# Performance work log

Measured on AMD Instinct MI355X. Metric: run time of the kernel, lower is better.

## Reference

```python
import jax, jax.numpy as jnp
import numpy as np
import math

N_HEADS = 16

def setup_inputs() -> dict:
    key = jax.random.key(0)
    ks = jax.random.split(key, 5)
    B, S, D = 4, 2048, 1024
    scale = 0.02
    return {
        "x": jax.random.normal(ks[0], (B, S, D), dtype=jnp.float32),
        "w_in": jax.random.normal(ks[1], (D, 3 * D), dtype=jnp.float32) * scale,
        "b_in": jax.random.normal(ks[2], (3 * D,), dtype=jnp.float32) * scale,
        "w_out": jax.random.normal(ks[3], (D, D), dtype=jnp.float32) * scale,
        "b_out": jax.random.normal(ks[4], (D,), dtype=jnp.float32) * scale,
    }

def reference(x, w_in, b_in, w_out, b_out):
    B, S, D = x.shape
    H = N_HEADS
    dh = D // H
    qkv = x @ w_in + b_in                      # [B,S,3D]
    q, k, v = jnp.split(qkv, 3, axis=-1)
    # [B,S,D] -> [B,H,S,dh]
    q = q.reshape(B, S, H, dh).transpose(0, 2, 1, 3)
    k = k.reshape(B, S, H, dh).transpose(0, 2, 1, 3)
    v = v.reshape(B, S, H, dh).transpose(0, 2, 1, 3)
    scores = jnp.einsum("bhqd,bhkd->bhqk", q, k) / math.sqrt(dh)
    causal = jnp.tril(jnp.ones((S, S), dtype=bool))  # allow k <= q
    scores = jnp.where(causal, scores, -jnp.inf)
    wei = jax.nn.softmax(scores, axis=-1)
    out = jnp.einsum("bhqk,bhkd->bhqd", wei, v)      # [B,H,S,dh]
    out = out.transpose(0, 2, 1, 3).reshape(B, S, D)
    return out @ w_out + b_out
```

## Files before the change

kernel.cpp:

```cpp
#include <hip/hip_runtime.h>

typedef unsigned short u16;
typedef unsigned int   u32;
typedef float  f32x4  __attribute__((ext_vector_type(4)));
typedef __bf16 bf16x8 __attribute__((ext_vector_type(8)));
typedef __bf16 bf16x4 __attribute__((ext_vector_type(4)));
typedef short  s16x4  __attribute__((ext_vector_type(4)));
typedef unsigned short u16x8 __attribute__((ext_vector_type(8)));
typedef unsigned int   u32x4 __attribute__((ext_vector_type(4)));

__device__ __forceinline__ u16 f2bf(float f) {
  u32 u = __builtin_bit_cast(u32, f);
  u = (u + 0x7fffu + ((u >> 16) & 1u)) >> 16;
  return (u16)u;
}

__device__ __forceinline__ void gload_lds16(const void* g, void* l) {
  __builtin_amdgcn_global_load_lds(
      (const __attribute__((address_space(1))) void*)g,
      (__attribute__((address_space(3))) void*)l, 16, 0, 0);
}

#define LGKM0()  asm volatile("s_waitcnt lgkmcnt(0)" ::: "memory")
#define VMCNT6() asm volatile("s_waitcnt vmcnt(6)" ::: "memory")
#define VMCNT0() asm volatile("s_waitcnt vmcnt(0)" ::: "memory")

__global__ __launch_bounds__(256) void conv_f32_bf16(
    const float* __restrict__ in, u16* __restrict__ out, int n8) {
  int i = blockIdx.x * 256 + threadIdx.x;
  if (i >= n8) return;
  const float4* p = (const float4*)in;
  float4 a = p[2 * i], b = p[2 * i + 1];
  u16x8 r;
  r[0] = f2bf(a.x); r[1] = f2bf(a.y); r[2] = f2bf(a.z); r[3] = f2bf(a.w);
  r[4] = f2bf(b.x); r[5] = f2bf(b.y); r[6] = f2bf(b.z); r[7] = f2bf(b.w);
  ((u16x8*)out)[i] = r;
}

__global__ __launch_bounds__(256) void conv_transpose(
    const float* __restrict__ in, u16* __restrict__ out, int K, int N) {
  __shared__ float tile[64][65];
  int nb = N >> 6;
  int tk = blockIdx.x / nb, tn = blockIdx.x % nb;
  int t = threadIdx.x;
  int kl = t >> 4, n4 = (t & 15) * 4;
#pragma unroll
  for (int i = 0; i < 4; ++i) {
    int k = kl + 16 * i;
    float4 v = *(const float4*)(in + (size_t)(tk * 64 + k) * N + tn * 64 + n4);
    tile[k][n4] = v.x; tile[k][n4 + 1] = v.y; tile[k][n4 + 2] = v.z; tile[k][n4 + 3] = v.w;
  }
  __syncthreads();
  int nl = t >> 4, k4 = (t & 15) * 4;
#pragma unroll
  for (int i = 0; i < 4; ++i) {
    int n = nl + 16 * i;
    ushort4 o;
    o.x = f2bf(tile[k4 + 0][n]); o.y = f2bf(tile[k4 + 1][n]);
    o.z = f2bf(tile[k4 + 2][n]); o.w = f2bf(tile[k4 + 3][n]);
    *(ushort4*)(out + (size_t)(tn * 64 + n) * K + tk * 64 + k4) = o;
  }
}

template <int OUT_BF16, int SCALE_Q>
__global__ __launch_bounds__(512, 2) void gemm8p(
    const u16* __restrict__ A, const u16* __restrict__ Bt,
    const float* __restrict__ bias, void* __restrict__ C,
    int M, int N, int K) {
  __shared__ __align__(16) char smem[2][49152];
  int tid = threadIdx.x, w = tid >> 6, lane = tid & 63;
  int g = lane >> 4, l15 = lane & 15, l7 = lane & 7, l8 = lane >> 3;
  int wm = w >> 2, wn = w & 3;
  int cpx = (int)gridDim.x >> 3;
  int bid = (blockIdx.x & 7) * cpx + (blockIdx.x >> 3);
  int nblk = N >> 7;
  int bm = bid / nblk, bn = bid % nblk;
  int m0 = bm << 8, n0 = bn << 7;

  auto stageA = [&](int buf, int kt, int h) {
#pragma unroll
    for (int i = 0; i < 2; ++i) {
      int row = h * 128 + w * 16 + i * 8 + l8;
      const u16* src = A + (size_t)(m0 + row) * K + kt * 64 + 8 * (l7 ^ (row & 7));
      gload_lds16(src, &smem[buf][(h * 128 + w * 16 + i * 8) * 128]);
    }
  };
  auto stageB = [&](int buf, int kt, int h) {
    int row = h * 64 + w * 8 + l8;
    const u16* src = Bt + (size_t)(n0 + row) * K + kt * 64 + 8 * (l7 ^ (row & 7));
    gload_lds16(src, &smem[buf][32768 + (h * 64 + w * 8) * 128]);
  };
  auto ldA = [&](int buf, int mh, int mi, int kk) -> bf16x8 {
    int row = mh * 128 + wm * 64 + mi * 16 + l15;
    return *(const bf16x8*)&smem[buf][row * 128 + (((kk * 4 + g) * 16) ^ ((row & 7) << 4))];
  };
  auto ldB = [&](int buf, int nh, int kk) -> bf16x8 {
    int row = nh * 64 + wn * 16 + l15;
    return *(const bf16x8*)&smem[buf][32768 + row * 128 + (((kk * 4 + g) * 16) ^ ((row & 7) << 4))];
  };

  f32x4 acc[2][4][2];
#pragma unroll
  for (int mh = 0; mh < 2; ++mh)
#pragma unroll
    for (int mi = 0; mi < 4; ++mi)
#pragma unroll
      for (int nh = 0; nh < 2; ++nh) acc[mh][mi][nh] = f32x4{0.f, 0.f, 0.f, 0.f};

  const int NT = K >> 6;
#pragma unroll
  for (int t = 0; t < 2; ++t) {
    stageB(t, t, 0); stageA(t, t, 0); stageB(t, t, 1); stageA(t, t, 1);
  }
  VMCNT6();
  __builtin_amdgcn_s_barrier();

  for (int t = 0; t < NT; ++t) {
    int b = t & 1;
    bool pf = (t + 2) < NT;
    bf16x8 af[4][2], b0f[2], b1f[2];

#pragma unroll
    for (int mi = 0; mi < 4; ++mi)
#pragma unroll
      for (int kk = 0; kk < 2; ++kk) af[mi][kk] = ldA(b, 0, mi, kk);
#pragma unroll
    for (int kk = 0; kk < 2; ++kk) b0f[kk] = ldB(b, 0, kk);
    LGKM0();
    __builtin_amdgcn_s_barrier();
    if (pf) stageB(b, t + 2, 0);
    __builtin_amdgcn_s_setprio(1);
#pragma unroll
    for (int mi = 0; mi < 4; ++mi)
#pragma unroll
      for (int kk = 0; kk < 2; ++kk)
        acc[0][mi][0] = __builtin_amdgcn_mfma_f32_16x16x32_bf16(af[mi][kk], b0f[kk], acc[0][mi][0], 0, 0, 0);
    __builtin_amdgcn_s_setprio(0);

#pragma unroll
    for (int kk = 0; kk < 2; ++kk) b1f[kk] = ldB(b, 1, kk);
    LGKM0();
    __builtin_amdgcn_s_barrier();
    if (pf) stageA(b, t + 2, 0);
    __builtin_amdgcn_s_setprio(1);
#pragma unroll
    for (int mi = 0; mi < 4; ++mi)
#pragma unroll
      for (int kk = 0; kk < 2; ++kk)
        acc[0][mi][1] = __builtin_amdgcn_mfma_f32_16x16x32_bf16(af[mi][kk], b1f[kk], acc[0][mi][1], 0, 0, 0);
    __builtin_amdgcn_s_setprio(0);

#pragma unroll
    for (int mi = 0; mi < 4; ++mi)
#pragma unroll
      for (int kk = 0; kk < 2; ++kk) af[mi][kk] = ldA(b, 1, mi, kk);
    LGKM0();
    __builtin_amdgcn_s_barrier();
    if (pf) stageB(b, t + 2, 1);
    __builtin_amdgcn_s_setprio(1);
#pragma unroll
    for (int mi = 0; mi < 4; ++mi)
#pragma unroll
      for (int kk = 0; kk < 2; ++kk)
        acc[1][mi][1] = __builtin_amdgcn_mfma_f32_16x16x32_bf16(af[mi][kk], b1f[kk], acc[1][mi][1], 0, 0, 0);
    __builtin_amdgcn_s_setprio(0);

    if (pf) stageA(b, t + 2, 1);
    __builtin_amdgcn_s_setprio(1);
#pragma unroll
    for (int mi = 0; mi < 4; ++mi)
#pragma unroll
      for (int kk = 0; kk < 2; ++kk)
        acc[1][mi][0] = __builtin_amdgcn_mfma_f32_16x16x32_bf16(af[mi][kk], b0f[kk], acc[1][mi][0], 0, 0, 0);
    __builtin_amdgcn_s_setprio(0);

    if (t < NT - 1) {
      if (pf) VMCNT6(); else VMCNT0();
      __builtin_amdgcn_s_barrier();
    }
  }

#pragma unroll
  for (int nh = 0; nh < 2; ++nh) {
    int col = n0 + nh * 64 + wn * 16 + l15;
    float bv = bias[col];
    float sc = (SCALE_Q && col < 1024) ? 0.18033688011112042f : 1.0f;
#pragma unroll
    for (int mh = 0; mh < 2; ++mh)
#pragma unroll
      for (int mi = 0; mi < 4; ++mi) {
        int rowb = m0 + mh * 128 + wm * 64 + mi * 16 + g * 4;
#pragma unroll
        for (int r = 0; r < 4; ++r) {
          float v = (acc[mh][mi][nh][r] + bv) * sc;
          if (OUT_BF16)
            ((u16*)C)[(size_t)(rowb + r) * N + col] = f2bf(v);
          else
            ((float*)C)[(size_t)(rowb + r) * N + col] = v;
        }
      }
  }
}


#if __has_builtin(__builtin_amdgcn_mfma_f32_16x16x16bf16_1k)
#define HAVE_MFMA16 1
__device__ __forceinline__ f32x4 mfma16(s16x4 a, s16x4 b, f32x4 c) {
  return __builtin_amdgcn_mfma_f32_16x16x16bf16_1k(a, b, c, 0, 0, 0);
}
#endif

struct V2reg { u16x8 a, b; };

__device__ __forceinline__ void stage_k(const u16* qb, char* kbuf, int kvt,
                                        int h, int w, int lane) {
  int l7 = lane & 7;
#pragma unroll
  for (int i = 0; i < 2; ++i) {
    int rbase = w * 16 + i * 8;
    int row = rbase + (lane >> 3);
    const u16* src = qb + (size_t)(kvt * 64 + row) * 3072 + 1024 + h * 64 + 8 * (l7 ^ (row & 7));
    gload_lds16(src, kbuf + rbase * 128);
  }
}

__device__ __forceinline__ V2reg load_v(const u16* qb, int kvt, int h, int kv0, int d0) {
  const u16* vs = qb + (size_t)(kvt * 64 + kv0) * 3072 + 2048 + h * 64 + d0;
  V2reg r;
  r.a = *(const u16x8*)vs;
  r.b = *(const u16x8*)(vs + 3072);
  return r;
}

__device__ __forceinline__ void write_v(char* vbuf, V2reg v, int kv0, int d0) {
#pragma unroll
  for (int j = 0; j < 8; ++j) {
    int d = d0 + j;
    u32 val = (u32)v.a[j] | ((u32)v.b[j] << 16);
    int sw = ((d & 7) ^ (d >> 3)) << 4;
    *(u32*)(vbuf + d * 128 + ((2 * kv0) ^ sw)) = val;
  }
}

__global__ __launch_bounds__(256, 4) void attn_fwd(
    const u16* __restrict__ qkv, u16* __restrict__ aout) {
  const int S = 2048, D3 = 3072;
  int bh = blockIdx.x & 63;
  int qt = 31 - (blockIdx.x >> 6);
  int b = bh >> 4, h = bh & 15;
  const u16* qb = qkv + (size_t)b * S * D3;

  int tid = threadIdx.x;
  int w = tid >> 6, lane = tid & 63;
  int g = lane >> 4, l15 = lane & 15, l7 = lane & 7;

  __shared__ __align__(16) char Kb[2][8192];
  __shared__ __align__(16) char Vb[2][8192];

  int qrow = qt * 64 + w * 16 + l15;
  const u16* qp = qb + (size_t)qrow * D3 + h * 64 + g * 8;
  bf16x8 qf0 = *(const bf16x8*)qp;
  bf16x8 qf1 = *(const bf16x8*)(qp + 32);

  f32x4 oaT[4];
#pragma unroll
  for (int i = 0; i < 4; ++i) oaT[i] = f32x4{0.f, 0.f, 0.f, 0.f};
  f32x4 l_acc = {0.f, 0.f, 0.f, 0.f};
  float m_s = -3e38f;

  int vkv0 = w * 16 + ((lane >> 3) << 1);
  int vd0 = l7 * 8;

  stage_k(qb, Kb[0], 0, h, w, lane);
  {
    V2reg v = load_v(qb, 0, h, vkv0, vd0);
    write_v(Vb[0], v, vkv0, vd0);
  }
  __syncthreads();

  V2reg vreg;
  for (int kvt = 0; kvt <= qt; ++kvt) {
    int cur = kvt & 1;
    if (kvt < qt) {
      stage_k(qb, Kb[cur ^ 1], kvt + 1, h, w, lane);
      vreg = load_v(qb, kvt + 1, h, vkv0, vd0);
    }

    f32x4 sT[4];
    __builtin_amdgcn_s_setprio(1);
#pragma unroll
    for (int nb = 0; nb < 4; ++nb) {
      int kv = nb * 16 + l15;
      const char* kb = Kb[cur] + kv * 128;
      int sw = (kv & 7) << 4;
      bf16x8 kf0 = *(const bf16x8*)(kb + ((g * 16) ^ sw));
      bf16x8 kf1 = *(const bf16x8*)(kb + ((64 + g * 16) ^ sw));
      f32x4 z = {0.f, 0.f, 0.f, 0.f};
      z = __builtin_amdgcn_mfma_f32_16x16x32_bf16(kf0, qf0, z, 0, 0, 0);
      z = __builtin_amdgcn_mfma_f32_16x16x32_bf16(kf1, qf1, z, 0, 0, 0);
      sT[nb] = z;
    }
    __builtin_amdgcn_s_setprio(0);

    if (kvt == qt) {
      int qloc = w * 16 + l15;
#pragma unroll
      for (int nb = 0; nb < 4; ++nb)
#pragma unroll
        for (int r = 0; r < 4; ++r)
          if (nb * 16 + g * 4 + r > qloc) sT[nb][r] = -1e30f;
    }

    float pm = -3e38f;
#pragma unroll
    for (int nb = 0; nb < 4; ++nb)
#pragma unroll
      for (int r = 0; r < 4; ++r) pm = fmaxf(pm, sT[nb][r]);
    pm = fmaxf(pm, __shfl_xor(pm, 16));
    pm = fmaxf(pm, __shfl_xor(pm, 32));
    if (!__all(pm - m_s <= 8.0f)) {
      float newm = fmaxf(m_s, pm);
      float corr = __builtin_amdgcn_exp2f(m_s - newm);
      m_s = newm;
      l_acc[0] *= corr;
#pragma unroll
      for (int db = 0; db < 4; ++db)
#pragma unroll
        for (int r = 0; r < 4; ++r) oaT[db][r] *= corr;
    }
#pragma unroll
    for (int nb = 0; nb < 4; ++nb)
#pragma unroll
      for (int r = 0; r < 4; ++r)
        sT[nb][r] = __builtin_amdgcn_exp2f(sT[nb][r] - m_s);

#ifdef HAVE_MFMA16
    s16x4 pf[4];
#pragma unroll
    for (int nb = 0; nb < 4; ++nb) {
      bf16x4 t;
#pragma unroll
      for (int r = 0; r < 4; ++r) t[r] = (__bf16)sT[nb][r];
      pf[nb] = __builtin_bit_cast(s16x4, t);
    }
    s16x4 ones;
#pragma unroll
    for (int r = 0; r < 4; ++r) ones[r] = (short)0x3F80;
    __builtin_amdgcn_s_setprio(1);
#pragma unroll
    for (int nb = 0; nb < 4; ++nb) l_acc = mfma16(ones, pf[nb], l_acc);
#pragma unroll
    for (int db = 0; db < 4; ++db) {
      int d = db * 16 + l15;
      const char* vb = Vb[cur] + d * 128;
      int swd = ((d & 7) ^ (d >> 3)) << 4;
#pragma unroll
      for (int nb = 0; nb < 4; ++nb) {
        bf16x4 vf = *(const bf16x4*)(vb + ((nb * 32 + g * 8) ^ swd));
        oaT[db] = mfma16(__builtin_bit_cast(s16x4, vf), pf[nb], oaT[db]);
      }
    }
    __builtin_amdgcn_s_setprio(0);
#else
    u32 wlo[4], whi[4];
#pragma unroll
    for (int nb = 0; nb < 4; ++nb) {
      wlo[nb] = (u32)f2bf(sT[nb][0]) | ((u32)f2bf(sT[nb][1]) << 16);
      whi[nb] = (u32)f2bf(sT[nb][2]) | ((u32)f2bf(sT[nb][3]) << 16);
    }
    int srcA = (2 * (g & 1)) * 16 + l15;
    int srcB = srcA + 16;
    bool hi = (g >> 1) != 0;
    bf16x8 ones8;
#pragma unroll
    for (int j = 0; j < 8; ++j) ones8[j] = __builtin_bit_cast(__bf16, (u16)0x3F80);
    __builtin_amdgcn_s_setprio(1);
#pragma unroll
    for (int kb2 = 0; kb2 < 2; ++kb2) {
      int nbE = kb2 * 2, nbO = kb2 * 2 + 1;
      u32 a0 = __shfl(wlo[nbE], srcA), a1 = __shfl(whi[nbE], srcA);
      u32 a2 = __shfl(wlo[nbE], srcB), a3 = __shfl(whi[nbE], srcB);
      u32 b0 = __shfl(wlo[nbO], srcA), b1 = __shfl(whi[nbO], srcA);
      u32 b2 = __shfl(wlo[nbO], srcB), b3 = __shfl(whi[nbO], srcB);
      u32x4 ow = {hi ? b0 : a0, hi ? b1 : a1, hi ? b2 : a2, hi ? b3 : a3};
      bf16x8 pfrag = __builtin_bit_cast(bf16x8, ow);
      l_acc = __builtin_amdgcn_mfma_f32_16x16x32_bf16(ones8, pfrag, l_acc, 0, 0, 0);
#pragma unroll
      for (int db = 0; db < 4; ++db) {
        int d = db * 16 + l15;
        int swd = ((d & 7) ^ (d >> 3)) << 4;
        bf16x8 vf = *(const bf16x8*)(Vb[cur] + d * 128 + ((kb2 * 64 + g * 16) ^ swd));
        oaT[db] = __builtin_amdgcn_mfma_f32_16x16x32_bf16(vf, pfrag, oaT[db], 0, 0, 0);
      }
    }
    __builtin_amdgcn_s_setprio(0);
#endif

    if (kvt < qt) {
      write_v(Vb[cur ^ 1], vreg, vkv0, vd0);
      __syncthreads();
    }
  }

  float inv = 1.0f / l_acc[0];
  size_t obase = (size_t)(b * S + qt * 64 + w * 16 + l15) * 1024 + h * 64;
#pragma unroll
  for (int db = 0; db < 4; ++db) {
    ushort4 st;
    st.x = f2bf(oaT[db][0] * inv);
    st.y = f2bf(oaT[db][1] * inv);
    st.z = f2bf(oaT[db][2] * inv);
    st.w = f2bf(oaT[db][3] * inv);
    *(ushort4*)(aout + obase + db * 16 + g * 4) = st;
  }
}

extern "C" void kernel_launch(void* const* d_in, const int* in_sizes, int n_in,
                              void* d_out, int out_size, void* d_ws, size_t ws_size,
                              hipStream_t stream) {
  (void)in_sizes; (void)n_in; (void)out_size;
  const float* x     = (const float*)d_in[0];
  const float* w_in  = (const float*)d_in[1];
  const float* b_in  = (const float*)d_in[2];
  const float* w_out = (const float*)d_in[3];
  const float* b_out = (const float*)d_in[4];
  float* out = (float*)d_out;
  char* ws = (char*)d_ws;
  if (ws_size < 92274688u) return;

  u16* xb     = (u16*)(ws);
  u16* w_inT  = (u16*)(ws + (16u << 20));
  u16* w_outT = (u16*)(ws + (22u << 20));
  u16* qkv    = (u16*)(ws + (24u << 20));
  u16* aout   = (u16*)(ws + (72u << 20));

  conv_f32_bf16<<<4096, 256, 0, stream>>>(x, xb, 1048576);
  conv_transpose<<<768, 256, 0, stream>>>(w_in, w_inT, 1024, 3072);
  conv_transpose<<<256, 256, 0, stream>>>(w_out, w_outT, 1024, 1024);
  gemm8p<1, 1><<<768, 512, 0, stream>>>(xb, w_inT, b_in, qkv, 8192, 3072, 1024);
  attn_fwd<<<2048, 256, 0, stream>>>(qkv, aout);
  gemm8p<0, 0><<<256, 512, 0, stream>>>(aout, w_outT, b_out, out, 8192, 1024, 1024);
}
```

Baseline: 262.3 us.

## Switch GEMM to triple-buffered LDS pipeline with one barrier per k-tile

The GEMM moves from a double-buffered LDS scheme with four barriers and lgkmcnt waits per k-tile to a three-buffer ring. Each k-tile now needs one wait and barrier, then issues the prefetch two tiles ahead. The B fragment layout per wave changes to 32 contiguous columns. Shared memory grows to 144 KB per block, which can stop two blocks fitting per CU and reduce occupancy.

```diff
diff --git a/kernel.cpp b/kernel.cpp
--- a/kernel.cpp
+++ b/kernel.cpp
@@ -21,7 +21,6 @@
       (__attribute__((address_space(3))) void*)l, 16, 0, 0);
 }
 
-#define LGKM0()  asm volatile("s_waitcnt lgkmcnt(0)" ::: "memory")
 #define VMCNT6() asm volatile("s_waitcnt vmcnt(6)" ::: "memory")
 #define VMCNT0() asm volatile("s_waitcnt vmcnt(0)" ::: "memory")
 
@@ -63,11 +62,11 @@
 }
 
 template <int OUT_BF16, int SCALE_Q>
-__global__ __launch_bounds__(512, 2) void gemm8p(
+__global__ __launch_bounds__(512, 2) void gemm3b(
     const u16* __restrict__ A, const u16* __restrict__ Bt,
     const float* __restrict__ bias, void* __restrict__ C,
     int M, int N, int K) {
-  __shared__ __align__(16) char smem[2][49152];
+  __shared__ __align__(16) char smem[3][49152];
   int tid = threadIdx.x, w = tid >> 6, lane = tid & 63;
   int g = lane >> 4, l15 = lane & 15, l7 = lane & 7, l8 = lane >> 3;
   int wm = w >> 2, wn = w & 3;
@@ -77,25 +76,26 @@
   int bm = bid / nblk, bn = bid % nblk;
   int m0 = bm << 8, n0 = bn << 7;
 
-  auto stageA = [&](int buf, int kt, int h) {
+  auto stageAB = [&](int buf, int kt) {
+#pragma unroll
+    for (int i = 0; i < 4; ++i) {
+      int row = w * 32 + i * 8 + l8;
+      const u16* src = A + (size_t)(m0 + row) * K + kt * 64 + 8 * (l7 ^ (row & 7));
+      gload_lds16(src, &smem[buf][(w * 32 + i * 8) * 128]);
+    }
 #pragma unroll
     for (int i = 0; i < 2; ++i) {
-      int row = h * 128 + w * 16 + i * 8 + l8;
-      const u16* src = A + (size_t)(m0 + row) * K + kt * 64 + 8 * (l7 ^ (row & 7));
-      gload_lds16(src, &smem[buf][(h * 128 + w * 16 + i * 8) * 128]);
-    }
-  };
-  auto stageB = [&](int buf, int kt, int h) {
-    int row = h * 64 + w * 8 + l8;
-    const u16* src = Bt + (size_t)(n0 + row) * K + kt * 64 + 8 * (l7 ^ (row & 7));
-    gload_lds16(src, &smem[buf][32768 + (h * 64 + w * 8) * 128]);
+      int row = w * 16 + i * 8 + l8;
+      const u16* src = Bt + (size_t)(n0 + row) * K + kt * 64 + 8 * (l7 ^ (row & 7));
+      gload_lds16(src, &smem[buf][32768 + (w * 16 + i * 8) * 128]);
+    }
   };
   auto ldA = [&](int buf, int mh, int mi, int kk) -> bf16x8 {
     int row = mh * 128 + wm * 64 + mi * 16 + l15;
     return *(const bf16x8*)&smem[buf][row * 128 + (((kk * 4 + g) * 16) ^ ((row & 7) << 4))];
   };
-  auto ldB = [&](int buf, int nh, int kk) -> bf16x8 {
-    int row = nh * 64 + wn * 16 + l15;
+  auto ldB = [&](int buf, int ni, int kk) -> bf16x8 {
+    int row = wn * 32 + ni * 16 + l15;
     return *(const bf16x8*)&smem[buf][32768 + row * 128 + (((kk * 4 + g) * 16) ^ ((row & 7) << 4))];
   };
 
@@ -105,30 +105,28 @@
 #pragma unroll
     for (int mi = 0; mi < 4; ++mi)
 #pragma unroll
-      for (int nh = 0; nh < 2; ++nh) acc[mh][mi][nh] = f32x4{0.f, 0.f, 0.f, 0.f};
+      for (int ni = 0; ni < 2; ++ni) acc[mh][mi][ni] = f32x4{0.f, 0.f, 0.f, 0.f};
 
   const int NT = K >> 6;
-#pragma unroll
-  for (int t = 0; t < 2; ++t) {
-    stageB(t, t, 0); stageA(t, t, 0); stageB(t, t, 1); stageA(t, t, 1);
-  }
-  VMCNT6();
-  __builtin_amdgcn_s_barrier();
-
+  stageAB(0, 0);
+  stageAB(1, 1);
+
+  int rb = 0;
   for (int t = 0; t < NT; ++t) {
-    int b = t & 1;
-    bool pf = (t + 2) < NT;
+    if (t < NT - 1) VMCNT6(); else VMCNT0();
+    __builtin_amdgcn_s_barrier();
+    if (t + 2 < NT) {
+      int sb = rb + 2; if (sb >= 3) sb -= 3;
+      stageAB(sb, t + 2);
+    }
+
     bf16x8 af[4][2], b0f[2], b1f[2];
-
-#pragma unroll
-    for (int mi = 0; mi < 4; ++mi)
-#pragma unroll
-      for (int kk = 0; kk < 2; ++kk) af[mi][kk] = ldA(b, 0, mi, kk);
-#pragma unroll
-    for (int kk = 0; kk < 2; ++kk) b0f[kk] = ldB(b, 0, kk);
-    LGKM0();
-    __builtin_amdgcn_s_barrier();
-    if (pf) stageB(b, t + 2, 0);
+#pragma unroll
+    for (int mi = 0; mi < 4; ++mi)
+#pragma unroll
+      for (int kk = 0; kk < 2; ++kk) af[mi][kk] = ldA(rb, 0, mi, kk);
+#pragma unroll
+    for (int kk = 0; kk < 2; ++kk) b0f[kk] = ldB(rb, 0, kk);
     __builtin_amdgcn_s_setprio(1);
 #pragma unroll
     for (int mi = 0; mi < 4; ++mi)
@@ -136,12 +134,8 @@
       for (int kk = 0; kk < 2; ++kk)
         acc[0][mi][0] = __builtin_amdgcn_mfma_f32_16x16x32_bf16(af[mi][kk], b0f[kk], acc[0][mi][0], 0, 0, 0);
     __builtin_amdgcn_s_setprio(0);
-
-#pragma unroll
-    for (int kk = 0; kk < 2; ++kk) b1f[kk] = ldB(b, 1, kk);
-    LGKM0();
-    __builtin_amdgcn_s_barrier();
-    if (pf) stageA(b, t + 2, 0);
+#pragma unroll
+    for (int kk = 0; kk < 2; ++kk) b1f[kk] = ldB(rb, 1, kk);
     __builtin_amdgcn_s_setprio(1);
 #pragma unroll
     for (int mi = 0; mi < 4; ++mi)
@@ -149,14 +143,10 @@
       for (int kk = 0; kk < 2; ++kk)
         acc[0][mi][1] = __builtin_amdgcn_mfma_f32_16x16x32_bf16(af[mi][kk], b1f[kk], acc[0][mi][1], 0, 0, 0);
     __builtin_amdgcn_s_setprio(0);
-
-#pragma unroll
-    for (int mi = 0; mi < 4; ++mi)
-#pragma unroll
-      for (int kk = 0; kk < 2; ++kk) af[mi][kk] = ldA(b, 1, mi, kk);
-    LGKM0();
-    __builtin_amdgcn_s_barrier();
-    if (pf) stageB(b, t + 2, 1);
+#pragma unroll
+    for (int mi = 0; mi < 4; ++mi)
+#pragma unroll
+      for (int kk = 0; kk < 2; ++kk) af[mi][kk] = ldA(rb, 1, mi, kk);
     __builtin_amdgcn_s_setprio(1);
 #pragma unroll
     for (int mi = 0; mi < 4; ++mi)
@@ -164,8 +154,6 @@
       for (int kk = 0; kk < 2; ++kk)
         acc[1][mi][1] = __builtin_amdgcn_mfma_f32_16x16x32_bf16(af[mi][kk], b1f[kk], acc[1][mi][1], 0, 0, 0);
     __builtin_amdgcn_s_setprio(0);
-
-    if (pf) stageA(b, t + 2, 1);
     __builtin_amdgcn_s_setprio(1);
 #pragma unroll
     for (int mi = 0; mi < 4; ++mi)
@@ -174,15 +162,12 @@
         acc[1][mi][0] = __builtin_amdgcn_mfma_f32_16x16x32_bf16(af[mi][kk], b0f[kk], acc[1][mi][0], 0, 0, 0);
     __builtin_amdgcn_s_setprio(0);
 
-    if (t < NT - 1) {
-      if (pf) VMCNT6(); else VMCNT0();
-      __builtin_amdgcn_s_barrier();
-    }
-  }
-
-#pragma unroll
-  for (int nh = 0; nh < 2; ++nh) {
-    int col = n0 + nh * 64 + wn * 16 + l15;
+    ++rb; if (rb >= 3) rb -= 3;
+  }
+
+#pragma unroll
+  for (int ni = 0; ni < 2; ++ni) {
+    int col = n0 + wn * 32 + ni * 16 + l15;
     float bv = bias[col];
     float sc = (SCALE_Q && col < 1024) ? 0.18033688011112042f : 1.0f;
 #pragma unroll
@@ -192,7 +177,7 @@
         int rowb = m0 + mh * 128 + wm * 64 + mi * 16 + g * 4;
 #pragma unroll
         for (int r = 0; r < 4; ++r) {
-          float v = (acc[mh][mi][nh][r] + bv) * sc;
+          float v = (acc[mh][mi][ni][r] + bv) * sc;
           if (OUT_BF16)
             ((u16*)C)[(size_t)(rowb + r) * N + col] = f2bf(v);
           else
@@ -437,7 +422,7 @@
   conv_f32_bf16<<<4096, 256, 0, stream>>>(x, xb, 1048576);
   conv_transpose<<<768, 256, 0, stream>>>(w_in, w_inT, 1024, 3072);
   conv_transpose<<<256, 256, 0, stream>>>(w_out, w_outT, 1024, 1024);
-  gemm8p<1, 1><<<768, 512, 0, stream>>>(xb, w_inT, b_in, qkv, 8192, 3072, 1024);
+  gemm3b<1, 1><<<768, 512, 0, stream>>>(xb, w_inT, b_in, qkv, 8192, 3072, 1024);
   attn_fwd<<<2048, 256, 0, stream>>>(qkv, aout);
-  gemm8p<0, 0><<<256, 512, 0, stream>>>(aout, w_outT, b_out, out, 8192, 1024, 1024);
-}
+  gemm3b<0, 0><<<256, 512, 0, stream>>>(aout, w_outT, b_out, out, 8192, 1024, 1024);
+}
```

After: 257.1 us. 1.02x faster.
